# Performance work log

Measured on AMD Instinct MI355X. Metric: run time of the kernel, lower is better.

The kernel has to match this reference:

```python
import jax, jax.numpy as jnp
import numpy as np

B, Q, T, H, W = 8, 100, 50, 256, 256
COST_MASK_W = 1.0  # init kwarg cost_mask
COST_DICE_W = 1.0  # init kwarg cost_dice


def setup_inputs() -> dict:
    key = jax.random.key(0)
    k1, k2 = jax.random.split(key)
    pred_masks = jax.random.normal(k1, (B, Q, H, W), dtype=jnp.float32)
    # binary GT masks (0/1), already at prediction resolution so nearest-interp is identity
    tgt_masks = jax.random.randint(k2, (B, T, H, W), 0, 2).astype(jnp.int32)
    return {"pred_masks": pred_masks, "tgt_masks": tgt_masks}


def reference(pred_masks, tgt_masks):
    # pred_masks: [B, Q, H, W] logits; tgt_masks: [B, T, H, W] binary
    b, q = pred_masks.shape[:2]
    x = pred_masks.reshape(b, q, -1)                      # [B, Q, HW]
    t = tgt_masks.reshape(b, tgt_masks.shape[1], -1).astype(x.dtype)  # [B, T, HW]
    hw = x.shape[-1]

    # batch_sigmoid_ce_loss: BCE-with-logits vs all-ones / all-zeros targets
    pos = jax.nn.softplus(-x)                             # BCE(x, 1)
    neg = jax.nn.softplus(x)                              # BCE(x, 0)
    cost_ce = (jnp.einsum('bqc,btc->bqt', pos, t)
               + jnp.einsum('bqc,btc->bqt', neg, 1.0 - t)) / hw

    # batch_dice_loss
    s = jax.nn.sigmoid(x)
    numerator = 2.0 * jnp.einsum('bqc,btc->bqt', s, t)
    denominator = s.sum(-1)[:, :, None] + t.sum(-1)[:, None, :]
    cost_dice = 1.0 - (numerator + 1.0) / (denominator + 1.0)

    # per-batch cost matrix C [B, Q, T]; the scipy Hungarian step is a
    # host-side CPU call outside the accelerator workload.
    return COST_MASK_W * cost_ce + COST_DICE_W * cost_dice
```

## Files before the change

kernel.cpp:

```cpp
#include <hip/hip_runtime.h>
#include <hip/hip_bf16.h>
#include <math.h>

#define B_ 8
#define Q_ 100
#define T_ 50
#define HW_ 65536

#define PSEG3 64
#define SEG3 (HW_ / PSEG3)
#define NT3 (SEG3 / 32)
#define PF 2
#define PROWS 101
#define PCOLS 52
#define PTILE ((size_t)PROWS * PCOLS)
#define PBLK ((size_t)B_ * PTILE)
#define D2OFF3 ((size_t)PSEG3 * PBLK)
#define WS3_NEEDED_BYTES (2ull * D2OFF3 * 4ull)

#define NSEG 64
#define SEG (HW_ / NSEG)
#define NK32 (SEG / 32)
#define NSTR 52
#define DSZ (B_ * Q_ * NSTR)
#define WS_D1 0
#define WS_D2 DSZ
#define WS_SNEG (2 * DSZ)
#define WS_ST (2 * DSZ + B_ * Q_)
#define WS_TOTAL (2 * DSZ + B_ * Q_ + B_ * T_)

typedef __attribute__((ext_vector_type(8))) short bf16x8;
typedef __attribute__((ext_vector_type(4))) float f32x4;

__device__ __forceinline__ unsigned short f2bf(float f) {
    union { float f; unsigned u; } v; v.f = f;
    unsigned r = v.u + 0x7FFF + ((v.u >> 16) & 1);
    return (unsigned short)(r >> 16);
}

__device__ __forceinline__ unsigned pkbf(float a, float b) {
    float2 f2; f2.x = a; f2.y = b;
    __hip_bfloat162 h2 = __float22bfloat162_rn(f2);
    unsigned u; __builtin_memcpy(&u, &h2, 4); return u;
}

__device__ __forceinline__ void gld_lds16(const void* g, void* l) {
    __builtin_amdgcn_global_load_lds((const __attribute__((address_space(1))) void*)g,
                                     (__attribute__((address_space(3))) void*)l,
                                     16, 0, 0);
}

__global__ __launch_bounds__(512, 4) void gemm_fused_p3(const float* __restrict__ pred,
                                                        const int* __restrict__ tgt,
                                                        float* __restrict__ ws) {
    const int seg = blockIdx.x;
    const int b   = blockIdx.y;
    const int tid = threadIdx.x;
    const int wave = tid >> 6;
    const int lane = tid & 63;
    const int quad = lane >> 4;
    const int l16  = lane & 15;

    __shared__ float xs[PF][128 * 32];
    __shared__ int   tsh[PF][64 * 32];

    const int rA  = tid >> 3;
    const int rB  = rA + 64;
    const int cg  = (tid & 7) ^ (rA & 7);
    const int rBc = rB < Q_ ? rB : Q_ - 1;
    const int tnc = rA < T_ ? rA : T_ - 1;
    const float* gx0 = pred + ((size_t)b * Q_ + rA)  * HW_ + (size_t)seg * SEG3 + cg * 4;
    const float* gx1 = pred + ((size_t)b * Q_ + rBc) * HW_ + (size_t)seg * SEG3 + cg * 4;
    const int*   gt  = tgt  + ((size_t)b * T_ + tnc) * HW_ + (size_t)seg * SEG3 + cg * 4;

    auto stage = [&](int ch, int slot) {
        const int ko = ch * 32;
        gld_lds16(gx0 + ko, &xs[slot][wave * 256]);
        gld_lds16(gx1 + ko, &xs[slot][2048 + wave * 256]);
        gld_lds16(gt  + ko, &tsh[slot][wave * 256]);
    };

    f32x4 accx[4], accs[4];
#pragma unroll
    for (int nt = 0; nt < 4; ++nt) { accx[nt] = (f32x4)(0.f); accs[nt] = (f32x4)(0.f); }
    float sneg = 0.f;

    const int aones = (wave * 16 + l16) == Q_;
    const int srow  = l16 & 7;
    const int c0 = ((2 * quad)     ^ srow) * 4;
    const int c1 = ((2 * quad + 1) ^ srow) * 4;
    const int xrowoff = (wave * 16 + l16) * 32;

    stage(0, 0);
    stage(1, 1);

    int slot = 0;
    float4 xa, xb;
    int4 ta[4], tb[4];

    for (int ch = 0; ch < NT3; ++ch) {
        if (ch + 1 < NT3) asm volatile("s_waitcnt vmcnt(3)" ::: "memory");
        else              asm volatile("s_waitcnt vmcnt(0)" ::: "memory");
        asm volatile("s_barrier" ::: "memory");

        {
            const float* xr = &xs[slot][xrowoff];
            xa = *(const float4*)(xr + c0);
            xb = *(const float4*)(xr + c1);
#pragma unroll
            for (int nt = 0; nt < 4; ++nt) {
                const int* tr = &tsh[slot][(nt * 16 + l16) * 32];
                ta[nt] = *(const int4*)(tr + c0);
                tb[nt] = *(const int4*)(tr + c1);
            }
        }
        asm volatile("s_waitcnt lgkmcnt(0)" ::: "memory");
        __builtin_amdgcn_sched_barrier(0);
        asm volatile("s_barrier" ::: "memory");

        if (ch + PF < NT3) stage(ch + PF, slot);

        bf16x8 tf[4];
#pragma unroll
        for (int nt = 0; nt < 4; ++nt) {
            short base = ((nt * 16 + l16) == T_) ? (short)0x3F80 : (short)0;
#pragma unroll
            for (int e = 0; e < 4; ++e) {
                tf[nt][e]     = (&ta[nt].x)[e] ? (short)0x3F80 : base;
                tf[nt][4 + e] = (&tb[nt].x)[e] ? (short)0x3F80 : base;
            }
        }
        float xe[8] = {xa.x, xa.y, xa.z, xa.w, xb.x, xb.y, xb.z, xb.w};
        float sg8[8];
        float sp = 0.f;
#pragma unroll
        for (int e = 0; e < 8; ++e) {
            float x = xe[e];
            float ax = fabsf(x);
            float ee = __expf(-ax);
            float d = 1.f + ee;
            float r1 = __builtin_amdgcn_rcpf(d);
            sg8[e] = (x >= 0.f) ? r1 : ee * r1;
            sp += fmaxf(x, 0.f) + 0.69314718056f * __log2f(d);
        }
        sneg += sp;
        unsigned xu[4], su[4];
#pragma unroll
        for (int j = 0; j < 4; ++j) {
            xu[j] = aones ? 0x3F803F80u : pkbf(xe[2 * j], xe[2 * j + 1]);
            su[j] = aones ? 0x3F803F80u : pkbf(sg8[2 * j], sg8[2 * j + 1]);
        }
        bf16x8 xf, sf;
        __builtin_memcpy(&xf, xu, 16);
        __builtin_memcpy(&sf, su, 16);
#pragma unroll
        for (int nt = 0; nt < 4; ++nt) {
            accx[nt] = __builtin_amdgcn_mfma_f32_16x16x32_bf16(xf, tf[nt], accx[nt], 0, 0, 0);
            accs[nt] = __builtin_amdgcn_mfma_f32_16x16x32_bf16(sf, tf[nt], accs[nt], 0, 0, 0);
        }
        slot ^= 1;
    }

    float* d1 = ws + (size_t)(seg * B_ + b) * PTILE;
    float* d2 = d1 + D2OFF3;

    {
        float v = sneg;
        v += __shfl_xor(v, 16);
        v += __shfl_xor(v, 32);
        int m = wave * 16 + l16;
        if (quad == 0 && m < Q_) d1[(size_t)m * PCOLS + 51] = v;
    }
    const int mtile = wave * 16;
#pragma unroll
    for (int nt = 0; nt < 4; ++nt) {
        int n = nt * 16 + l16;
#pragma unroll
        for (int r = 0; r < 4; ++r) {
            int m = mtile + quad * 4 + r;
            if (m <= Q_ && n <= T_) {
                size_t idx = (size_t)m * PCOLS + n;
                d1[idx] = accx[nt][r];
                d2[idx] = accs[nt][r];
            }
        }
    }
}

__global__ void reduce_p3(float* __restrict__ ws) {
    int j = blockIdx.x * blockDim.x + threadIdx.x;
    const int Q4 = (int)(PBLK / 4);
    if (j >= 2 * Q4) return;
    int y = blockIdx.y;
    size_t off = (j < Q4) ? ((size_t)j * 4) : (D2OFF3 + (size_t)(j - Q4) * 4);
    const float4* p = (const float4*)(ws + off);
    int s0 = y * (PSEG3 / 4);
    float a0 = 0.f, a1 = 0.f, a2 = 0.f, a3 = 0.f;
#pragma unroll 4
    for (int s = s0; s < s0 + PSEG3 / 4; ++s) {
        float4 v = p[(size_t)s * (PBLK / 4)];
        a0 += v.x; a1 += v.y; a2 += v.z; a3 += v.w;
    }
    float4 r; r.x = a0; r.y = a1; r.z = a2; r.w = a3;
    *(float4*)(ws + off + (size_t)s0 * PBLK) = r;
}

__global__ void finalize_p3(const float* __restrict__ ws, float* __restrict__ out) {
    int i = blockIdx.x * blockDim.x + threadIdx.x;
    if (i >= B_ * Q_ * T_) return;
    int b = i / (Q_ * T_);
    int r = i % (Q_ * T_);
    int q = r / T_;
    int t = r % T_;
    float dx = 0.f, ds = 0.f, ss = 0.f, sn = 0.f, stv = 0.f;
#pragma unroll
    for (int y = 0; y < 4; ++y) {
        const float* d1 = ws + (size_t)y * (PSEG3 / 4) * PBLK + (size_t)b * PTILE;
        const float* d2 = d1 + D2OFF3;
        dx  += d1[(size_t)q * PCOLS + t];
        ds  += d2[(size_t)q * PCOLS + t];
        ss  += d2[(size_t)q * PCOLS + T_];
        sn  += d1[(size_t)q * PCOLS + 51];
        stv += d1[(size_t)Q_ * PCOLS + t];
    }
    float ce = (sn - dx) * (1.f / (float)HW_);
    float dice = 1.f - (2.f * ds + 1.f) / (ss + stv + 1.f);
    out[i] = ce + dice;
}

__global__ void zero_ws(float* ws) {
    int i = blockIdx.x * blockDim.x + threadIdx.x;
    if (i < WS_TOTAL) ws[i] = 0.f;
}

__global__ __launch_bounds__(256, 2) void gemm_fused(const float* __restrict__ pred,
                                                     const int* __restrict__ tgt,
                                                     float* __restrict__ ws) {
    const int seg = blockIdx.x;
    const int b   = blockIdx.y;
    const int tid = threadIdx.x;
    const int wave = tid >> 6;
    const int lane = tid & 63;
    const int quad = lane >> 4;
    const int l16  = lane & 15;

    const float* xptr[2];
#pragma unroll
    for (int mt = 0; mt < 2; ++mt) {
        int m = (wave + mt * 4) * 16 + l16;
        int mr = m < Q_ ? m : Q_ - 1;
        xptr[mt] = pred + ((size_t)b * Q_ + mr) * HW_ + (size_t)seg * SEG + quad * 8;
    }
    const int* tptr[4];
    int ones[4];
#pragma unroll
    for (int nt = 0; nt < 4; ++nt) {
        int n = nt * 16 + l16;
        ones[nt] = (n == T_);
        int nr = n < T_ ? n : T_ - 1;
        tptr[nt] = tgt + ((size_t)b * T_ + nr) * HW_ + (size_t)seg * SEG + quad * 8;
    }

    f32x4 accx[2][4], accs[2][4];
#pragma unroll
    for (int mt = 0; mt < 2; ++mt)
#pragma unroll
        for (int nt = 0; nt < 4; ++nt) {
            accx[mt][nt] = (f32x4)(0.f);
            accs[mt][nt] = (f32x4)(0.f);
        }
    float sneg[2] = {0.f, 0.f};
    float stq[4] = {0.f, 0.f, 0.f, 0.f};

    float4 xrb[2][2][2];
    int4   trb[2][4][2];

    auto loadraw = [&](int ch, float4 xr[2][2], int4 tr[4][2]) {
        const int k = ch * 32;
#pragma unroll
        for (int mt = 0; mt < 2; ++mt) {
            xr[mt][0] = *(const float4*)(xptr[mt] + k);
            xr[mt][1] = *(const float4*)(xptr[mt] + k + 4);
        }
#pragma unroll
        for (int nt = 0; nt < 4; ++nt) {
            tr[nt][0] = *(const int4*)(tptr[nt] + k);
            tr[nt][1] = *(const int4*)(tptr[nt] + k + 4);
        }
    };

    auto compute = [&](float4 xr[2][2], int4 tr[4][2]) {
        bf16x8 tf[4];
#pragma unroll
        for (int nt = 0; nt < 4; ++nt) {
            float cnt = 0.f;
#pragma unroll
            for (int h = 0; h < 2; ++h)
#pragma unroll
                for (int e = 0; e < 4; ++e) {
                    int v = (&tr[nt][h].x)[e];
                    tf[nt][h * 4 + e] = (v || ones[nt]) ? (short)0x3F80 : (short)0;
                    cnt += v ? 1.f : 0.f;
                }
            stq[nt] += cnt;
        }
#pragma unroll
        for (int mt = 0; mt < 2; ++mt) {
            bf16x8 xf, sf;
            float sp = 0.f;
#pragma unroll
            for (int h = 0; h < 2; ++h)
#pragma unroll
                for (int e = 0; e < 4; ++e) {
                    float x = (&xr[mt][h].x)[e];
                    float ax = fabsf(x);
                    float ee = __expf(-ax);
                    float d = 1.f + ee;
                    float r1 = __builtin_amdgcn_rcpf(d);
                    float sg = (x >= 0.f) ? r1 : ee * r1;
                    sp += fmaxf(x, 0.f) + 0.69314718056f * __log2f(d);
                    xf[h * 4 + e] = (short)f2bf(x);
                    sf[h * 4 + e] = (short)f2bf(sg);
                }
            sneg[mt] += sp;
#pragma unroll
            for (int nt = 0; nt < 4; ++nt) {
                accx[mt][nt] = __builtin_amdgcn_mfma_f32_16x16x32_bf16(xf, tf[nt], accx[mt][nt], 0, 0, 0);
                accs[mt][nt] = __builtin_amdgcn_mfma_f32_16x16x32_bf16(sf, tf[nt], accs[mt][nt], 0, 0, 0);
            }
        }
    };

    loadraw(0, xrb[0], trb[0]);
#pragma unroll 2
    for (int ch = 0; ch < NK32; ++ch) {
        const int cb = ch & 1;
        if (ch + 1 < NK32) loadraw(ch + 1, xrb[cb ^ 1], trb[cb ^ 1]);
        compute(xrb[cb], trb[cb]);
    }

#pragma unroll
    for (int mt = 0; mt < 2; ++mt) {
        float v = sneg[mt];
        v += __shfl_xor(v, 16);
        v += __shfl_xor(v, 32);
        int m = (wave + mt * 4) * 16 + l16;
        if (quad == 0 && m < Q_) atomicAdd(&ws[WS_SNEG + b * Q_ + m], v);
    }
    if (wave == 0) {
#pragma unroll
        for (int nt = 0; nt < 4; ++nt) {
            float v = stq[nt];
            v += __shfl_xor(v, 16);
            v += __shfl_xor(v, 32);
            int n = nt * 16 + l16;
            if (quad == 0 && n < T_) atomicAdd(&ws[WS_ST + b * T_ + n], v);
        }
    }
#pragma unroll
    for (int mt = 0; mt < 2; ++mt) {
        int mtile = (wave + mt * 4) * 16;
#pragma unroll
        for (int nt = 0; nt < 4; ++nt) {
            int n = nt * 16 + l16;
#pragma unroll
            for (int r = 0; r < 4; ++r) {
                int m = mtile + quad * 4 + r;
                if (m < Q_) {
                    size_t idx = ((size_t)b * Q_ + m) * NSTR + n;
                    if (n < T_) atomicAdd(&ws[WS_D1 + idx], accx[mt][nt][r]);
                    if (n <= T_) atomicAdd(&ws[WS_D2 + idx], accs[mt][nt][r]);
                }
            }
        }
    }
}

__global__ void finalize(const float* __restrict__ ws, float* __restrict__ out) {
    int i = blockIdx.x * blockDim.x + threadIdx.x;
    if (i >= B_ * Q_ * T_) return;
    int b = i / (Q_ * T_);
    int r = i % (Q_ * T_);
    int q = r / T_;
    int t = r % T_;
    float dx   = ws[WS_D1 + ((size_t)b * Q_ + q) * NSTR + t];
    float ds   = ws[WS_D2 + ((size_t)b * Q_ + q) * NSTR + t];
    float ssum = ws[WS_D2 + ((size_t)b * Q_ + q) * NSTR + T_];
    float st   = ws[WS_ST + b * T_ + t];
    float sneg = ws[WS_SNEG + b * Q_ + q];
    float ce = (sneg - dx) * (1.f / (float)HW_);
    float dice = 1.f - (2.f * ds + 1.f) / (ssum + st + 1.f);
    out[i] = ce + dice;
}

extern "C" void kernel_launch(void* const* d_in, const int* in_sizes, int n_in,
                              void* d_out, int out_size, void* d_ws, size_t ws_size,
                              hipStream_t stream) {
    const float* pred = (const float*)d_in[0];
    const int* tgt = (const int*)d_in[1];
    float* ws = (float*)d_ws;
    float* out = (float*)d_out;

    if (ws_size >= WS3_NEEDED_BYTES) {
        dim3 g(PSEG3, B_, 1);
        gemm_fused_p3<<<g, 512, 0, stream>>>(pred, tgt, ws);
        const int Q4 = (int)(PBLK / 4);
        dim3 rg((2 * Q4 + 255) / 256, 4, 1);
        reduce_p3<<<rg, 256, 0, stream>>>(ws);
        finalize_p3<<<(B_ * Q_ * T_ + 255) / 256, 256, 0, stream>>>(ws, out);
    } else {
        zero_ws<<<(WS_TOTAL + 255) / 256, 256, 0, stream>>>(ws);
        dim3 g(NSEG, B_, 1);
        gemm_fused<<<g, 256, 0, stream>>>(pred, tgt, ws);
        finalize<<<(B_ * Q_ * T_ + 255) / 256, 256, 0, stream>>>(ws, out);
    }
}
```

Measured before the change: 393.5 us.

## Pack binary targets into bitmasks and feed MFMA directly from bits

Adds a pre-pass that ballot-packs the int32 target masks into a bitmask buffer in the workspace, including an all-ones row used for the target sums. A new GEMM kernel loads the packed bits and expands them into bf16 operand fragments in registers, with no LDS staging. The grid is also split over two query halves. The goal is to cut target-mask memory traffic by about 32x per read, at the cost of one extra full read of the int32 targets in the pack pass and a larger workspace requirement.

```diff
diff --git a/kernel.cpp b/kernel.cpp
--- a/kernel.cpp
+++ b/kernel.cpp
@@ -18,6 +18,10 @@
 #define D2OFF3 ((size_t)PSEG3 * PBLK)
 #define WS3_NEEDED_BYTES (2ull * D2OFF3 * 4ull)
 
+#define BITS_WORDS (B_ * 64 * 2048)
+#define BITS_FOFF (2 * D2OFF3)
+#define WS6_NEEDED_BYTES ((2ull * D2OFF3 + (unsigned long long)BITS_WORDS) * 4ull)
+
 #define NSEG 64
 #define SEG (HW_ / NSEG)
 #define NK32 (SEG / 32)
@@ -42,6 +46,143 @@
     float2 f2; f2.x = a; f2.y = b;
     __hip_bfloat162 h2 = __float22bfloat162_rn(f2);
     unsigned u; __builtin_memcpy(&u, &h2, 4); return u;
+}
+
+#define PACK_GROUPS (B_ * 64 * (HW_ / 64))
+__global__ __launch_bounds__(256) void pack_t(const int* __restrict__ tgt,
+                                              unsigned* __restrict__ bits) {
+    int wid = (blockIdx.x * blockDim.x + threadIdx.x) >> 6;
+    int lane = threadIdx.x & 63;
+    int nw = (gridDim.x * blockDim.x) >> 6;
+    for (int g = wid; g < PACK_GROUPS; g += nw) {
+        int b = g >> 16;
+        int row = (g >> 10) & 63;
+        int kbase = (g & 1023) << 6;
+        int v;
+        if (row < T_) v = tgt[((size_t)b * T_ + row) * HW_ + kbase + lane];
+        else v = (row == T_) ? 1 : 0;
+        unsigned long long mask = __ballot(v != 0);
+        size_t widx = ((size_t)(b * 64 + row) << 11) + (kbase >> 5);
+        if (lane == 0) bits[widx] = (unsigned)mask;
+        if (lane == 32) bits[widx + 1] = (unsigned)(mask >> 32);
+    }
+}
+
+__global__ __launch_bounds__(256, 4) void gemm_fused_p4(const float* __restrict__ pred,
+                                                        const unsigned* __restrict__ bits,
+                                                        float* __restrict__ ws) {
+    const int seg = blockIdx.x;
+    const int mh  = blockIdx.y;
+    const int b   = blockIdx.z;
+    const int tid = threadIdx.x;
+    const int wave = tid >> 6;
+    const int lane = tid & 63;
+    const int quad = lane >> 4;
+    const int l16  = lane & 15;
+
+    const int mrow = mh * 64 + wave * 16 + l16;
+    const int aones = (mrow == Q_);
+    const int mr = mrow < Q_ ? mrow : Q_ - 1;
+    const float* xptr = pred + ((size_t)b * Q_ + mr) * HW_ + (size_t)seg * SEG3 + quad * 8;
+
+    const unsigned* wp[4];
+#pragma unroll
+    for (int nt = 0; nt < 4; ++nt) {
+        int n = nt * 16 + l16;
+        wp[nt] = bits + ((size_t)(b * 64 + n) << 11) + (size_t)seg * NT3;
+    }
+
+    f32x4 accx[4], accs[4];
+#pragma unroll
+    for (int nt = 0; nt < 4; ++nt) { accx[nt] = (f32x4)(0.f); accs[nt] = (f32x4)(0.f); }
+    float sneg = 0.f;
+
+    float4   xrb[2][2];
+    unsigned wrb[2][4];
+
+    auto loadraw = [&](int ch, float4 xr[2], unsigned wr[4]) {
+#pragma unroll
+        for (int nt = 0; nt < 4; ++nt) wr[nt] = wp[nt][ch];
+        const int k = ch * 32;
+        xr[0] = *(const float4*)(xptr + k);
+        xr[1] = *(const float4*)(xptr + k + 4);
+    };
+
+    auto compute = [&](float4 xr[2], unsigned wr[4]) {
+        bf16x8 tf[4];
+#pragma unroll
+        for (int nt = 0; nt < 4; ++nt) {
+            unsigned mw = (wr[nt] >> (quad << 3)) & 0xFFu;
+            unsigned uu[4];
+#pragma unroll
+            for (int j = 0; j < 4; ++j) {
+                uu[j] = ((mw & 1u) * 0x3F80u) | (((mw & 2u) * 0x3F80u) << 15);
+                mw >>= 2;
+            }
+            __builtin_memcpy(&tf[nt], uu, 16);
+        }
+        float xe[8] = {xr[0].x, xr[0].y, xr[0].z, xr[0].w,
+                       xr[1].x, xr[1].y, xr[1].z, xr[1].w};
+        float sg8[8];
+        float sp = 0.f;
+#pragma unroll
+        for (int e = 0; e < 8; ++e) {
+            float x = xe[e];
+            float ax = fabsf(x);
+            float ee = __expf(-ax);
+            float d = 1.f + ee;
+            float r1 = __builtin_amdgcn_rcpf(d);
+            sg8[e] = (x >= 0.f) ? r1 : ee * r1;
+            sp += fmaxf(x, 0.f) + 0.69314718056f * __log2f(d);
+        }
+        sneg += sp;
+        unsigned xu[4], su[4];
+#pragma unroll
+        for (int j = 0; j < 4; ++j) {
+            xu[j] = aones ? 0x3F803F80u : pkbf(xe[2 * j], xe[2 * j + 1]);
+            su[j] = aones ? 0x3F803F80u : pkbf(sg8[2 * j], sg8[2 * j + 1]);
+        }
+        bf16x8 xf, sf;
+        __builtin_memcpy(&xf, xu, 16);
+        __builtin_memcpy(&sf, su, 16);
+#pragma unroll
+        for (int nt = 0; nt < 4; ++nt) {
+            accx[nt] = __builtin_amdgcn_mfma_f32_16x16x32_bf16(xf, tf[nt], accx[nt], 0, 0, 0);
+            accs[nt] = __builtin_amdgcn_mfma_f32_16x16x32_bf16(sf, tf[nt], accs[nt], 0, 0, 0);
+        }
+    };
+
+    loadraw(0, xrb[0], wrb[0]);
+#pragma unroll 2
+    for (int ch = 0; ch < NT3; ++ch) {
+        const int cb = ch & 1;
+        if (ch + 1 < NT3) loadraw(ch + 1, xrb[cb ^ 1], wrb[cb ^ 1]);
+        compute(xrb[cb], wrb[cb]);
+    }
+
+    float* d1 = ws + (size_t)(seg * B_ + b) * PTILE;
+    float* d2 = d1 + D2OFF3;
+
+    {
+        float v = sneg;
+        v += __shfl_xor(v, 16);
+        v += __shfl_xor(v, 32);
+        if (quad == 0 && mrow < Q_) d1[(size_t)mrow * PCOLS + 51] = v;
+    }
+    const int mtile = mh * 64 + wave * 16;
+#pragma unroll
+    for (int nt = 0; nt < 4; ++nt) {
+        int n = nt * 16 + l16;
+#pragma unroll
+        for (int r = 0; r < 4; ++r) {
+            int m = mtile + quad * 4 + r;
+            if (m <= Q_ && n <= T_) {
+                size_t idx = (size_t)m * PCOLS + n;
+                d1[idx] = accx[nt][r];
+                d2[idx] = accs[nt][r];
+            }
+        }
+    }
 }
 
 __device__ __forceinline__ void gld_lds16(const void* g, void* l) {
@@ -401,11 +542,19 @@
     float* ws = (float*)d_ws;
     float* out = (float*)d_out;
 
-    if (ws_size >= WS3_NEEDED_BYTES) {
+    const int Q4 = (int)(PBLK / 4);
+    dim3 rg((2 * Q4 + 255) / 256, 4, 1);
+
+    if (ws_size >= WS6_NEEDED_BYTES) {
+        unsigned* bits = (unsigned*)(ws + BITS_FOFF);
+        pack_t<<<2048, 256, 0, stream>>>(tgt, bits);
+        dim3 g(PSEG3, 2, B_);
+        gemm_fused_p4<<<g, 256, 0, stream>>>(pred, bits, ws);
+        reduce_p3<<<rg, 256, 0, stream>>>(ws);
+        finalize_p3<<<(B_ * Q_ * T_ + 255) / 256, 256, 0, stream>>>(ws, out);
+    } else if (ws_size >= WS3_NEEDED_BYTES) {
         dim3 g(PSEG3, B_, 1);
         gemm_fused_p3<<<g, 512, 0, stream>>>(pred, tgt, ws);
-        const int Q4 = (int)(PBLK / 4);
-        dim3 rg((2 * Q4 + 255) / 256, 4, 1);
         reduce_p3<<<rg, 256, 0, stream>>>(ws);
         finalize_p3<<<(B_ * Q_ * T_ + 255) / 256, 256, 0, stream>>>(ws, out);
     } else {
```

Result: slower. 445.4 us (+13.2%).
